# Kernel optimization log

Measured on AMD Instinct MI355X. Metric: run time of the kernel, lower is better.

Reference implementation:

```python
import jax, jax.numpy as jnp
import numpy as np

NUM_NODES = 51681
EMBED_DIM = 32
HIDDEN_DIM = 64
NUM_EDGES = 2048  # input_dim == edge_weight.size(0)


def gcn_conv(x, W, b, src, dst, edge_weight, num_nodes):
    """PyG GCNConv with add_self_loops=True, symmetric normalization.
    x: [N, Fin], W: [Fin, Fout], b: [Fout], src/dst: [E], edge_weight: [E].
    """
    loop = jnp.arange(num_nodes)
    row = jnp.concatenate([src, loop])            # source of message
    col = jnp.concatenate([dst, loop])            # target (aggregation) node
    w = jnp.concatenate([edge_weight, jnp.ones((num_nodes,), x.dtype)])
    deg = jax.ops.segment_sum(w, col, num_segments=num_nodes)   # [N]
    dinv = jnp.where(deg > 0, jax.lax.rsqrt(deg), 0.0)
    norm = dinv[row] * w * dinv[col]              # [E+N]
    xw = x @ W                                    # [N, Fout]
    msgs = norm[:, None] * xw[row]                # gather + scale
    out = jax.ops.segment_sum(msgs, col, num_segments=num_nodes)
    return out + b


def setup_inputs() -> dict:
    key = jax.random.key(0)
    ks = jax.random.split(key, 12)
    edge_index = jax.random.randint(ks[0], (2, NUM_EDGES), 0, NUM_NODES)
    edge_weight = jax.random.uniform(ks[1], (NUM_EDGES,), dtype=jnp.float32)
    embedding = jax.random.normal(ks[2], (NUM_NODES, EMBED_DIM), jnp.float32)
    def lin(k, fin, fout):
        return jax.random.normal(k, (fin, fout), jnp.float32) / np.sqrt(fin)
    return {
        "edge_index": edge_index,
        "edge_weight": edge_weight,
        "embedding": embedding,
        "enc_W1": lin(ks[3], EMBED_DIM, HIDDEN_DIM),
        "enc_b1": jnp.zeros((HIDDEN_DIM,), jnp.float32),
        "enc_W2": lin(ks[4], HIDDEN_DIM, EMBED_DIM),
        "enc_b2": jnp.zeros((EMBED_DIM,), jnp.float32),
        "dec_W1": lin(ks[5], EMBED_DIM, HIDDEN_DIM),
        "dec_b1": jnp.zeros((HIDDEN_DIM,), jnp.float32),
        "dec_W2": lin(ks[6], HIDDEN_DIM, NUM_EDGES),
        "dec_b2": jnp.zeros((NUM_EDGES,), jnp.float32),
    }


def reference(edge_index, edge_weight, embedding,
              enc_W1, enc_b1, enc_W2, enc_b2,
              dec_W1, dec_b1, dec_W2, dec_b2):
    src, dst = edge_index[0], edge_index[1]
    # Encoder
    x = jax.nn.relu(gcn_conv(embedding, enc_W1, enc_b1, src, dst, edge_weight, NUM_NODES))
    z = jax.nn.relu(gcn_conv(x, enc_W2, enc_b2, src, dst, edge_weight, NUM_NODES))
    # Decoder
    h = jax.nn.relu(gcn_conv(z, dec_W1, dec_b1, src, dst, edge_weight, NUM_NODES))
    recon_x = gcn_conv(h, dec_W2, dec_b2, src, dst, edge_weight, NUM_NODES)
    return recon_x, z
```

## Files before the change

kernel.cpp:

```cpp
#include <hip/hip_runtime.h>

#define NN 51681
#define EE 2048
#define Z_OFF (51681LL * 2048LL)

typedef __bf16 bf16x8 __attribute__((ext_vector_type(8)));
typedef unsigned short ushort8 __attribute__((ext_vector_type(8)));
typedef float floatx4 __attribute__((ext_vector_type(4)));

__device__ inline unsigned short f2bf(float x) {
    unsigned u = __float_as_uint(x);
    unsigned r = (u + 0x7FFFu + ((u >> 16) & 1u)) >> 16;
    return (unsigned short)r;
}
__device__ inline void nt_store4(float* p, floatx4 v) {
    __builtin_nontemporal_store(v, reinterpret_cast<floatx4*>(p));
}


__global__ void init_k(const float* __restrict__ W4,
                       ushort* __restrict__ wthi,
                       float* __restrict__ deg, const int* __restrict__ dst,
                       float* __restrict__ E4) {
    int b = blockIdx.x, t = threadIdx.x;
    if (b < 512) {
        int i = b * 256 + t;
        int k = i >> 11, c = i & 2047;
        wthi[c * 64 + k] = f2bf(W4[i]);
    } else if (b < 714) {
        int i = (b - 512) * 256 + t;
        if (i < NN) deg[i] = 1.0f;
    } else {
        int j = (b - 714) * 256 + t;
        int e = j >> 4, f = j & 15;
        reinterpret_cast<float4*>(&E4[(long long)dst[e] * 64])[f] =
            make_float4(0.f, 0.f, 0.f, 0.f);
    }
}

__global__ void deg_scatter_k(const int* __restrict__ dst, const float* __restrict__ w,
                              float* __restrict__ deg) {
    int e = blockIdx.x * 256 + threadIdx.x;
    if (e < EE) atomicAdd(&deg[dst[e]], w[e]);
}


__global__ void edge_scatter_k(const int* __restrict__ src, const int* __restrict__ dst,
                               const float* __restrict__ ew, const float* __restrict__ deg,
                               const float* __restrict__ X, float* __restrict__ E) {
    int tid = blockIdx.x * 256 + threadIdx.x;
    if (tid >= EE * 16) return;
    int e = tid >> 4;
    int f = (tid & 15) * 4;
    int s = src[e], d = dst[e];
    float n = rsqrtf(deg[s]) * ew[e] * rsqrtf(deg[d]);
    const float4 v = *reinterpret_cast<const float4*>(&X[(long long)s * 64 + f]);
    float* a = &E[(long long)d * 64 + f];
    atomicAdd(a + 0, n * v.x);
    atomicAdd(a + 1, n * v.y);
    atomicAdd(a + 2, n * v.z);
    atomicAdd(a + 3, n * v.w);
}


template<int K, int FOUT>
__global__ __launch_bounds__(256) void gemm_fused_k(
    const float* __restrict__ X,
    const int* __restrict__ src, const int* __restrict__ dst,
    const float* __restrict__ ew, const float* __restrict__ deg,
    const float* __restrict__ W, const float* __restrict__ bias,
    float* __restrict__ out) {
    constexpr int TPN = FOUT / 4;
    constexpr int NPB = 256 / TPN;
    __shared__ float Ws[K * FOUT];
    __shared__ float As[NPB][K + 4];
    __shared__ int qidx[EE];
    __shared__ int qcount;
    int tid = threadIdx.x;
    if (tid == 0) qcount = 0;
    for (int i = tid; i < K * FOUT / 4; i += 256)
        reinterpret_cast<float4*>(Ws)[i] = reinterpret_cast<const float4*>(W)[i];
    int node0 = blockIdx.x * NPB;
    for (int i = tid; i < NPB * (K / 4); i += 256) {
        int r = i / (K / 4);
        int kk = (i - r * (K / 4)) * 4;
        int g = node0 + r;
        float4 v = make_float4(0.f, 0.f, 0.f, 0.f);
        if (g < NN) {
            float s = 1.0f / deg[g];
            float4 xv = *reinterpret_cast<const float4*>(&X[(long long)g * K + kk]);
            v = make_float4(xv.x * s, xv.y * s, xv.z * s, xv.w * s);
        }
        *reinterpret_cast<float4*>(&As[r][kk]) = v;
    }
    __syncthreads();
    for (int e = tid; e < EE; e += 256) {
        unsigned r = (unsigned)(dst[e] - node0);
        if (r < (unsigned)NPB) { int s = atomicAdd(&qcount, 1); qidx[s] = e; }
    }
    __syncthreads();
    int nq = qcount;
    for (int qi = 0; qi < nq; ++qi) {
        int e = qidx[qi];
        int s_ = src[e], d_ = dst[e];
        float c = ew[e] * rsqrtf(deg[s_]) * rsqrtf(deg[d_]);
        int r = d_ - node0;
        if (tid < K) As[r][tid] += c * X[(long long)s_ * K + tid];
    }
    __syncthreads();
    int ln = tid / TPN;
    int n4 = (tid - ln * TPN) * 4;
    int g = node0 + ln;
    if (g >= NN) return;
    float4 acc = *reinterpret_cast<const float4*>(&bias[n4]);
    #pragma unroll
    for (int k = 0; k < K; ++k) {
        float a = As[ln][k];
        float4 w = *reinterpret_cast<const float4*>(&Ws[k * FOUT + n4]);
        acc.x = fmaf(a, w.x, acc.x);
        acc.y = fmaf(a, w.y, acc.y);
        acc.z = fmaf(a, w.z, acc.z);
        acc.w = fmaf(a, w.w, acc.w);
    }
    acc.x = fmaxf(acc.x, 0.f); acc.y = fmaxf(acc.y, 0.f);
    acc.z = fmaxf(acc.z, 0.f); acc.w = fmaxf(acc.w, 0.f);
    *reinterpret_cast<float4*>(&out[(long long)g * FOUT + n4]) = acc;
}


__global__ __launch_bounds__(512, 2) void gemm_big_k(
    const float* __restrict__ E, const float* __restrict__ H,
    const float* __restrict__ deg,
    const ushort* __restrict__ wthi,
    const float* __restrict__ bias, float* __restrict__ out) {
    __shared__ ushort Whi[256 * 64];
    int tid  = threadIdx.x;
    int lane = tid & 63;
    int wv   = tid >> 6;
    int rl   = lane & 15;
    int kg   = lane >> 4;
    int cbase = blockIdx.x * 256;
    int node  = blockIdx.y * 128 + wv * 16 + rl;
    bool valid = node < NN;

    {
        const ushort8* sh8 = reinterpret_cast<const ushort8*>(wthi + (size_t)cbase * 64);
        #pragma unroll
        for (int i = tid; i < 2048; i += 512) {
            int col = i >> 3, slot = i & 7;
            int d = col * 8 + (slot ^ (col & 7));
            reinterpret_cast<ushort8*>(Whi)[d] = sh8[i];
        }
    }

    floatx4 acc[16];
    #pragma unroll
    for (int tl = 0; tl < 16; ++tl)
        acc[tl] = *reinterpret_cast<const floatx4*>(&bias[cbase + tl * 16 + kg * 4]);

    bf16x8 nb_hi[2], nb_lo[2];
    {
        float v[2][8];
        if (valid) {
            float dg = deg[node];
            float s = 1.0f / dg;
            const float* h0 = H + (long long)node * 64 + kg * 8;
            #pragma unroll
            for (int f = 0; f < 2; ++f) {
                float4 ha = *reinterpret_cast<const float4*>(h0 + f * 32);
                float4 hb = *reinterpret_cast<const float4*>(h0 + f * 32 + 4);
                v[f][0] = ha.x * s; v[f][1] = ha.y * s; v[f][2] = ha.z * s; v[f][3] = ha.w * s;
                v[f][4] = hb.x * s; v[f][5] = hb.y * s; v[f][6] = hb.z * s; v[f][7] = hb.w * s;
            }
            if (dg != 1.0f) {
                const float* e0 = E + (long long)node * 64 + kg * 8;
                #pragma unroll
                for (int f = 0; f < 2; ++f) {
                    float4 ea = *reinterpret_cast<const float4*>(e0 + f * 32);
                    float4 eb = *reinterpret_cast<const float4*>(e0 + f * 32 + 4);
                    v[f][0] += ea.x; v[f][1] += ea.y; v[f][2] += ea.z; v[f][3] += ea.w;
                    v[f][4] += eb.x; v[f][5] += eb.y; v[f][6] += eb.z; v[f][7] += eb.w;
                }
            }
        } else {
            #pragma unroll
            for (int f = 0; f < 2; ++f)
                #pragma unroll
                for (int i = 0; i < 8; ++i) v[f][i] = 0.f;
        }
        #pragma unroll
        for (int f = 0; f < 2; ++f) {
            ushort8 h8, l8;
            #pragma unroll
            for (int i = 0; i < 8; ++i) {
                unsigned u = __float_as_uint(v[f][i]) & 0xFFFF0000u;
                h8[i] = (unsigned short)(u >> 16);
                l8[i] = f2bf(v[f][i] - __uint_as_float(u));
            }
            nb_hi[f] = __builtin_bit_cast(bf16x8, h8);
            nb_lo[f] = __builtin_bit_cast(bf16x8, l8);
        }
    }

    __syncthreads();

    #pragma unroll
    for (int tl = 0; tl < 16; ++tl) {
        int col  = tl * 16 + rl;
        int base = col * 64;
        int s0 = (kg ^ (rl & 7)) * 8;
        int s1 = ((kg + 4) ^ (rl & 7)) * 8;
        bf16x8 wh0 = *reinterpret_cast<const bf16x8*>(&Whi[base + s0]);
        bf16x8 wh1 = *reinterpret_cast<const bf16x8*>(&Whi[base + s1]);
        acc[tl] = __builtin_amdgcn_mfma_f32_16x16x32_bf16(wh0, nb_hi[0], acc[tl], 0, 0, 0);
        acc[tl] = __builtin_amdgcn_mfma_f32_16x16x32_bf16(wh0, nb_lo[0], acc[tl], 0, 0, 0);
        acc[tl] = __builtin_amdgcn_mfma_f32_16x16x32_bf16(wh1, nb_hi[1], acc[tl], 0, 0, 0);
        acc[tl] = __builtin_amdgcn_mfma_f32_16x16x32_bf16(wh1, nb_lo[1], acc[tl], 0, 0, 0);
    }

    __syncthreads();

    float* stg = reinterpret_cast<float*>(Whi);
    int rowbase = blockIdx.y * 128 + wv * 16;
    int sseg = lane >> 2, sj = lane & 3;
    #pragma unroll
    for (int round = 0; round < 4; ++round) {
        if ((wv >> 1) == round) {
            float* patch = stg + (wv & 1) * 4096;
            #pragma unroll
            for (int tl = 0; tl < 16; ++tl) {
                int w = rl * 256 + ((tl ^ rl) & 15) * 16 + kg * 4;
                *reinterpret_cast<floatx4*>(&patch[w]) = acc[tl];
            }
            #pragma unroll
            for (int r = 0; r < 16; ++r) {
                int w = r * 256 + ((sseg ^ r) & 15) * 16 + sj * 4;
                floatx4 v = *reinterpret_cast<const floatx4*>(&patch[w]);
                int gr = rowbase + r;
                if (gr < NN)
                    nt_store4(&out[(long long)gr * 2048 + cbase + lane * 4], v);
            }
        }
        __syncthreads();
    }
}


extern "C" void kernel_launch(void* const* d_in, const int* in_sizes, int n_in,
                              void* d_out, int out_size, void* d_ws, size_t ws_size,
                              hipStream_t stream) {
    const int*   edge_index = (const int*)d_in[0];
    const int*   src = edge_index;
    const int*   dst = edge_index + EE;
    const float* ew  = (const float*)d_in[1];
    const float* emb = (const float*)d_in[2];
    const float* W1  = (const float*)d_in[3];
    const float* b1  = (const float*)d_in[4];
    const float* W2  = (const float*)d_in[5];
    const float* b2  = (const float*)d_in[6];
    const float* W3  = (const float*)d_in[7];
    const float* b3  = (const float*)d_in[8];
    const float* W4  = (const float*)d_in[9];
    const float* b4  = (const float*)d_in[10];

    float* out = (float*)d_out;
    float* z   = out + Z_OFF;

    float* ws   = (float*)d_ws;
    float* deg  = ws;
    float* E4   = ws + 51712;
    float* t1   = E4 + 3307584;
    ushort* wthi = (ushort*)(t1 + 3307584);

    init_k<<<842, 256, 0, stream>>>(W4, wthi, deg, dst, E4);
    deg_scatter_k<<<(EE + 255) / 256, 256, 0, stream>>>(dst, ew, deg);

    gemm_fused_k<32, 64><<<(NN + 15) / 16, 256, 0, stream>>>(
        emb, src, dst, ew, deg, W1, b1, t1);

    gemm_fused_k<64, 32><<<(NN + 31) / 32, 256, 0, stream>>>(
        t1, src, dst, ew, deg, W2, b2, z);

    gemm_fused_k<32, 64><<<(NN + 15) / 16, 256, 0, stream>>>(
        z, src, dst, ew, deg, W3, b3, t1);

    edge_scatter_k<<<(EE * 16 + 255) / 256, 256, 0, stream>>>(src, dst, ew, deg, t1, E4);
    gemm_big_k<<<dim3(8, 404), 512, 0, stream>>>(E4, t1, deg, wthi, b4, out);
}
```

Before: 152.6 us.

## Fuse final-layer edge aggregation into big GEMM via per-block edge queue

Removes the separate edge_scatter kernel and the E4 zeroing pass in init. Each gemm_big_k block now scans all 2048 edges, queues those whose destination falls in its 128-row tile in shared memory, and each thread gathers its incoming neighbour rows directly from H. This saves one kernel launch and the atomic scatter traffic. In exchange, each of the ~3200 blocks scans the full edge list and runs an extra sync and a serial queue loop before the MFMA work, with the queue scan repeated across the 8 column blocks.

```diff
diff --git a/kernel.cpp b/kernel.cpp
--- a/kernel.cpp
+++ b/kernel.cpp
@@ -20,21 +20,15 @@
 
 __global__ void init_k(const float* __restrict__ W4,
                        ushort* __restrict__ wthi,
-                       float* __restrict__ deg, const int* __restrict__ dst,
-                       float* __restrict__ E4) {
+                       float* __restrict__ deg) {
     int b = blockIdx.x, t = threadIdx.x;
     if (b < 512) {
         int i = b * 256 + t;
         int k = i >> 11, c = i & 2047;
         wthi[c * 64 + k] = f2bf(W4[i]);
-    } else if (b < 714) {
+    } else {
         int i = (b - 512) * 256 + t;
         if (i < NN) deg[i] = 1.0f;
-    } else {
-        int j = (b - 714) * 256 + t;
-        int e = j >> 4, f = j & 15;
-        reinterpret_cast<float4*>(&E4[(long long)dst[e] * 64])[f] =
-            make_float4(0.f, 0.f, 0.f, 0.f);
     }
 }
 
@@ -42,24 +36,6 @@
                               float* __restrict__ deg) {
     int e = blockIdx.x * 256 + threadIdx.x;
     if (e < EE) atomicAdd(&deg[dst[e]], w[e]);
-}
-
-
-__global__ void edge_scatter_k(const int* __restrict__ src, const int* __restrict__ dst,
-                               const float* __restrict__ ew, const float* __restrict__ deg,
-                               const float* __restrict__ X, float* __restrict__ E) {
-    int tid = blockIdx.x * 256 + threadIdx.x;
-    if (tid >= EE * 16) return;
-    int e = tid >> 4;
-    int f = (tid & 15) * 4;
-    int s = src[e], d = dst[e];
-    float n = rsqrtf(deg[s]) * ew[e] * rsqrtf(deg[d]);
-    const float4 v = *reinterpret_cast<const float4*>(&X[(long long)s * 64 + f]);
-    float* a = &E[(long long)d * 64 + f];
-    atomicAdd(a + 0, n * v.x);
-    atomicAdd(a + 1, n * v.y);
-    atomicAdd(a + 2, n * v.z);
-    atomicAdd(a + 3, n * v.w);
 }
 
 
@@ -129,19 +105,26 @@
 
 
 __global__ __launch_bounds__(512, 2) void gemm_big_k(
-    const float* __restrict__ E, const float* __restrict__ H,
-    const float* __restrict__ deg,
+    const float* __restrict__ H, const float* __restrict__ deg,
+    const int* __restrict__ src, const int* __restrict__ dst,
+    const float* __restrict__ ew,
     const ushort* __restrict__ wthi,
     const float* __restrict__ bias, float* __restrict__ out) {
     __shared__ ushort Whi[256 * 64];
+    __shared__ int qidx[EE];
+    __shared__ int qcount;
     int tid  = threadIdx.x;
     int lane = tid & 63;
     int wv   = tid >> 6;
     int rl   = lane & 15;
     int kg   = lane >> 4;
     int cbase = blockIdx.x * 256;
-    int node  = blockIdx.y * 128 + wv * 16 + rl;
+    int node0 = blockIdx.y * 128;
+    int myrow = wv * 16 + rl;
+    int node  = node0 + myrow;
     bool valid = node < NN;
+
+    if (tid == 0) qcount = 0;
 
     {
         const ushort8* sh8 = reinterpret_cast<const ushort8*>(wthi + (size_t)cbase * 64);
@@ -152,6 +135,14 @@
             reinterpret_cast<ushort8*>(Whi)[d] = sh8[i];
         }
     }
+    __syncthreads();
+
+    for (int e = tid; e < EE; e += 512) {
+        unsigned r = (unsigned)(dst[e] - node0);
+        if (r < 128u) { int s = atomicAdd(&qcount, 1); qidx[s] = e; }
+    }
+    __syncthreads();
+    int nq = qcount;
 
     floatx4 acc[16];
     #pragma unroll
@@ -162,8 +153,7 @@
     {
         float v[2][8];
         if (valid) {
-            float dg = deg[node];
-            float s = 1.0f / dg;
+            float s = 1.0f / deg[node];
             const float* h0 = H + (long long)node * 64 + kg * 8;
             #pragma unroll
             for (int f = 0; f < 2; ++f) {
@@ -172,21 +162,29 @@
                 v[f][0] = ha.x * s; v[f][1] = ha.y * s; v[f][2] = ha.z * s; v[f][3] = ha.w * s;
                 v[f][4] = hb.x * s; v[f][5] = hb.y * s; v[f][6] = hb.z * s; v[f][7] = hb.w * s;
             }
-            if (dg != 1.0f) {
-                const float* e0 = E + (long long)node * 64 + kg * 8;
-                #pragma unroll
-                for (int f = 0; f < 2; ++f) {
-                    float4 ea = *reinterpret_cast<const float4*>(e0 + f * 32);
-                    float4 eb = *reinterpret_cast<const float4*>(e0 + f * 32 + 4);
-                    v[f][0] += ea.x; v[f][1] += ea.y; v[f][2] += ea.z; v[f][3] += ea.w;
-                    v[f][4] += eb.x; v[f][5] += eb.y; v[f][6] += eb.z; v[f][7] += eb.w;
-                }
-            }
         } else {
             #pragma unroll
             for (int f = 0; f < 2; ++f)
                 #pragma unroll
                 for (int i = 0; i < 8; ++i) v[f][i] = 0.f;
+        }
+        for (int qi = 0; qi < nq; ++qi) {
+            int e = qidx[qi];
+            int d_ = dst[e];
+            if (d_ - node0 == myrow) {
+                int s_ = src[e];
+                float c = ew[e] * rsqrtf(deg[s_]) * rsqrtf(deg[d_]);
+                const float* hs = H + (long long)s_ * 64 + kg * 8;
+                #pragma unroll
+                for (int f = 0; f < 2; ++f) {
+                    float4 ea = *reinterpret_cast<const float4*>(hs + f * 32);
+                    float4 eb = *reinterpret_cast<const float4*>(hs + f * 32 + 4);
+                    v[f][0] += c * ea.x; v[f][1] += c * ea.y;
+                    v[f][2] += c * ea.z; v[f][3] += c * ea.w;
+                    v[f][4] += c * eb.x; v[f][5] += c * eb.y;
+                    v[f][6] += c * eb.z; v[f][7] += c * eb.w;
+                }
+            }
         }
         #pragma unroll
         for (int f = 0; f < 2; ++f) {
@@ -201,8 +199,6 @@
             nb_lo[f] = __builtin_bit_cast(bf16x8, l8);
         }
     }
-
-    __syncthreads();
 
     #pragma unroll
     for (int tl = 0; tl < 16; ++tl) {
@@ -221,7 +217,7 @@
     __syncthreads();
 
     float* stg = reinterpret_cast<float*>(Whi);
-    int rowbase = blockIdx.y * 128 + wv * 16;
+    int rowbase = node0 + wv * 16;
     int sseg = lane >> 2, sj = lane & 3;
     #pragma unroll
     for (int round = 0; round < 4; ++round) {
@@ -268,11 +264,10 @@
 
     float* ws   = (float*)d_ws;
     float* deg  = ws;
-    float* E4   = ws + 51712;
-    float* t1   = E4 + 3307584;
+    float* t1   = ws + 51712;
     ushort* wthi = (ushort*)(t1 + 3307584);
 
-    init_k<<<842, 256, 0, stream>>>(W4, wthi, deg, dst, E4);
+    init_k<<<714, 256, 0, stream>>>(W4, wthi, deg);
     deg_scatter_k<<<(EE + 255) / 256, 256, 0, stream>>>(dst, ew, deg);
 
     gemm_fused_k<32, 64><<<(NN + 15) / 16, 256, 0, stream>>>(
@@ -284,6 +279,5 @@
     gemm_fused_k<32, 64><<<(NN + 15) / 16, 256, 0, stream>>>(
         z, src, dst, ew, deg, W3, b3, t1);
 
-    edge_scatter_k<<<(EE * 16 + 255) / 256, 256, 0, stream>>>(src, dst, ew, deg, t1, E4);
-    gemm_big_k<<<dim3(8, 404), 512, 0, stream>>>(E4, t1, deg, wthi, b4, out);
-}
+    gemm_big_k<<<dim3(8, 404), 512, 0, stream>>>(t1, deg, src, dst, ew, wthi, b4, out);
+}
```

New measurement: 156.4 us. 1.03x slower.
